# Kernel optimization log

Measured on AMD Instinct MI355X. Metric: run time of the kernel, lower is better.

Reference implementation:

```python
import jax, jax.numpy as jnp
import numpy as np

FEAT = 64
NSPIX = 256

def setup_inputs() -> dict:
    key = jax.random.key(0)
    ks = jax.random.split(key, 10)
    B, H, W = 8, 512, 512
    x = jax.random.normal(ks[0], (B, 3, H, W), dtype=jnp.float32)
    labels = jax.random.randint(ks[1], (B, 1, H, W), 0, NSPIX, dtype=jnp.int32)
    # learned params (1x1 convs as dense matrices, eval-mode BatchNorm stats)
    W_pix = jax.random.normal(ks[2], (FEAT, 3), dtype=jnp.float32) * 0.1
    b_pix = jax.random.normal(ks[3], (FEAT,), dtype=jnp.float32) * 0.01
    W_red = jax.random.normal(ks[4], (FEAT, 2 * FEAT), dtype=jnp.float32) * 0.05
    b_red = jax.random.normal(ks[5], (FEAT,), dtype=jnp.float32) * 0.01
    w_sim = jax.random.normal(ks[6], (1,), dtype=jnp.float32)
    b_sim = jax.random.normal(ks[7], (1,), dtype=jnp.float32) * 0.01
    bn_gamma = jnp.ones((1,), dtype=jnp.float32)
    bn_beta = jnp.zeros((1,), dtype=jnp.float32)
    bn_mean = jnp.zeros((1,), dtype=jnp.float32)
    bn_var = jnp.ones((1,), dtype=jnp.float32)
    return {"x": x, "labels": labels, "num_spixels": NSPIX,
            "W_pix": W_pix, "b_pix": b_pix, "W_red": W_red, "b_red": b_red,
            "w_sim": w_sim, "b_sim": b_sim,
            "bn_gamma": bn_gamma, "bn_beta": bn_beta,
            "bn_mean": bn_mean, "bn_var": bn_var}


def reference(x, labels, num_spixels, W_pix, b_pix, W_red, b_red,
              w_sim, b_sim, bn_gamma, bn_beta, bn_mean, bn_var):
    B, C, H, W = x.shape
    Fdim = W_pix.shape[0]
    # pixel_conv: 1x1 conv == per-pixel dense
    feats = jnp.einsum('fc,bchw->bfhw', W_pix, x) + b_pix[None, :, None, None]
    feats = feats.reshape(B, Fdim, H * W)              # [B, F, HW]
    lab = labels.reshape(B, H * W).astype(jnp.int32)   # [B, HW]
    # fused per-batch segment reduce: offset labels so one segment_sum handles all B
    seg = (lab + jnp.arange(B, dtype=jnp.int32)[:, None] * num_spixels).reshape(-1)
    nseg = B * num_spixels
    feat_flat = feats.transpose(0, 2, 1).reshape(-1, Fdim)       # [B*HW, F]
    count = jax.ops.segment_sum(jnp.ones((B * H * W,), dtype=feats.dtype), seg,
                                num_segments=nseg)
    count = jnp.maximum(count, 1.0).reshape(B, num_spixels, 1)    # [B, S, 1]
    ssum = jax.ops.segment_sum(feat_flat, seg, num_segments=nseg).reshape(B, num_spixels, Fdim)
    ssq = jax.ops.segment_sum(feat_flat * feat_flat, seg, num_segments=nseg).reshape(B, num_spixels, Fdim)
    mean = ssum / count                                           # [B, S, F]
    var = ssq / count - mean * mean
    std = jnp.sqrt(jnp.maximum(var, 1e-6))
    combined = jnp.concatenate([mean, std], axis=-1)              # [B, S, 2F]
    # reduce_conv: 1x1 conv over channel dim
    reduced = jnp.einsum('fg,bsg->bsf', W_red, combined) + b_red  # [B, S, F]
    # F.normalize(p=2, dim=channel) with eps=1e-12
    nrm = jnp.maximum(jnp.sqrt(jnp.sum(reduced * reduced, axis=-1, keepdims=True)), 1e-12)
    rn = reduced / nrm
    sim = jnp.einsum('bsf,btf->bst', rn, rn)                      # [B, S, S]
    # similarity_weight_block: Conv2d(1,1,1) -> BatchNorm2d(1, eval) -> ReLU
    y = sim * w_sim[0] + b_sim[0]
    y = bn_gamma[0] * (y - bn_mean[0]) / jnp.sqrt(bn_var[0] + 1e-5) + bn_beta[0]
    y = jax.nn.relu(y)
    return y[:, None, :, :]                                       # [B, 1, S, S]
```

## Files before the change

kernel.cpp:

```cpp
#include <hip/hip_runtime.h>

#define HW   262144
#define HW4  65536
#define NSEG 256
#define NB   8

__global__ __launch_bounds__(256) void k_moments(const float* __restrict__ x,
                                                 const int* __restrict__ labels,
                                                 float* __restrict__ part) {
  __shared__ unsigned cnt[NSEG];
  __shared__ unsigned offs[NSEG];
  __shared__ unsigned wtot[4];
  __shared__ __align__(16) float buf[2048][4];
  const int t = threadIdx.x, w = t >> 6, lane = t & 63;
  const int b = blockIdx.x >> 7, blk = blockIdx.x & 127;

  cnt[t] = 0u;
  __syncthreads();

  const float4* __restrict__ x4 = (const float4*)(x + (size_t)b * 3 * HW);
  const int4*  __restrict__ l4  = (const int4*)(labels + (size_t)b * HW);

  float4 A0[2], A1[2], A2[2];
  int lb[8];
  unsigned rk[8];

  #pragma unroll
  for (int it = 0; it < 2; ++it) {
    const int g = blk * 512 + w * 128 + it * 64 + lane;
    A0[it] = x4[g];
    A1[it] = x4[HW4 + g];
    A2[it] = x4[2 * HW4 + g];
    int4 lv = l4[g];
    lb[it * 4 + 0] = lv.x; lb[it * 4 + 1] = lv.y;
    lb[it * 4 + 2] = lv.z; lb[it * 4 + 3] = lv.w;
  }

  #pragma unroll
  for (int k = 0; k < 8; ++k) rk[k] = atomicAdd(&cnt[lb[k]], 1u);
  __syncthreads();

  const unsigned v = cnt[t];
  unsigned inc = v;
  #pragma unroll
  for (int off = 1; off < 64; off <<= 1) {
    unsigned u = __shfl_up(inc, off, 64);
    if (lane >= off) inc += u;
  }
  if (lane == 63) wtot[w] = inc;
  __syncthreads();
  unsigned wbase = 0;
  #pragma unroll
  for (int i = 0; i < 3; ++i) if (i < w) wbase += wtot[i];
  offs[t] = wbase + inc - v;
  __syncthreads();

  #pragma unroll
  for (int it = 0; it < 2; ++it) {
    float c0[4] = {A0[it].x, A0[it].y, A0[it].z, A0[it].w};
    float c1[4] = {A1[it].x, A1[it].y, A1[it].z, A1[it].w};
    float c2[4] = {A2[it].x, A2[it].y, A2[it].z, A2[it].w};
    #pragma unroll
    for (int k = 0; k < 4; ++k) {
      const int p = it * 4 + k;
      const unsigned pos = offs[lb[p]] + rk[p];
      *(float4*)&buf[pos][0] = make_float4(c0[k], c1[k], c2[k], 0.f);
    }
  }
  __syncthreads();

  const unsigned n = cnt[t], base = offs[t];
  float s0 = 0.f, s1 = 0.f, s2 = 0.f;
  float q00 = 0.f, q11 = 0.f, q22 = 0.f, q01 = 0.f, q02 = 0.f, q12 = 0.f;
  for (unsigned i = 0; i < n; ++i) {
    float4 p = *(const float4*)&buf[base + i][0];
    s0 += p.x;  s1 += p.y;  s2 += p.z;
    q00 += p.x * p.x;  q11 += p.y * p.y;  q22 += p.z * p.z;
    q01 += p.x * p.y;  q02 += p.x * p.z;  q12 += p.y * p.z;
  }

  float* o = part + (size_t)blockIdx.x * 2560;
  o[0 * NSEG + t] = (float)n;
  o[1 * NSEG + t] = s0;   o[2 * NSEG + t] = s1;   o[3 * NSEG + t] = s2;
  o[4 * NSEG + t] = q00;  o[5 * NSEG + t] = q11;  o[6 * NSEG + t] = q22;
  o[7 * NSEG + t] = q01;  o[8 * NSEG + t] = q02;  o[9 * NSEG + t] = q12;
}

__global__ __launch_bounds__(256) void k_reduce(const float* __restrict__ part,
                                                float* __restrict__ acc) {
  const int bm = blockIdx.x >> 2, c = blockIdx.x & 3;
  const int b = bm / 10, m = bm % 10;
  const float* p = part + ((size_t)(b * 128 + c * 32)) * 2560 + m * 256 + threadIdx.x;
  float s0 = 0.f, s1 = 0.f, s2 = 0.f, s3 = 0.f;
  for (int i = 0; i < 32; i += 4) {
    s0 += p[(size_t)(i + 0) * 2560];
    s1 += p[(size_t)(i + 1) * 2560];
    s2 += p[(size_t)(i + 2) * 2560];
    s3 += p[(size_t)(i + 3) * 2560];
  }
  acc[(size_t)((b * 4 + c) * 10 + m) * 256 + threadIdx.x] = (s0 + s1) + (s2 + s3);
}

__global__ __launch_bounds__(256) void k_stats(const float* __restrict__ acc,
                                               const float* __restrict__ W_pix,
                                               const float* __restrict__ b_pix,
                                               const float* __restrict__ W_red,
                                               const float* __restrict__ b_red,
                                               float* __restrict__ rn) {
  __shared__ float wred[64 * 129];
  __shared__ float comb[4][132];
  const int t = threadIdx.x;

  for (int j4 = t; j4 < 2048; j4 += 256) {
    const int row = j4 >> 5;
    const int c4  = (j4 & 31) << 2;
    float4 v = ((const float4*)W_red)[j4];
    float* d = &wred[row * 129 + c4];
    d[0] = v.x; d[1] = v.y; d[2] = v.z; d[3] = v.w;
  }
  __syncthreads();

  const int w = t >> 6;
  const int f = t & 63;
  const int seg = blockIdx.x * 4 + w;
  const int b = seg >> 8;
  const int s = seg & 255;

  float mm[10];
  #pragma unroll
  for (int m = 0; m < 10; ++m) {
    float v = 0.f;
    #pragma unroll
    for (int c = 0; c < 4; ++c)
      v += acc[(size_t)((b * 4 + c) * 10 + m) * 256 + s];
    mm[m] = v;
  }
  const float N   = fmaxf(mm[0], 1.0f);
  const float S0  = mm[1], S1 = mm[2], S2 = mm[3];
  const float M00 = mm[4], M11 = mm[5], M22 = mm[6];
  const float M01 = mm[7], M02 = mm[8], M12 = mm[9];

  const float w0 = W_pix[f * 3 + 0];
  const float w1 = W_pix[f * 3 + 1];
  const float w2 = W_pix[f * 3 + 2];
  const float bf = b_pix[f];

  const float wS   = w0 * S0 + w1 * S1 + w2 * S2;
  const float mean = (wS + N * bf) / N;
  const float ssq  = w0 * w0 * M00 + w1 * w1 * M11 + w2 * w2 * M22
                   + 2.f * (w0 * w1 * M01 + w0 * w2 * M02 + w1 * w2 * M12)
                   + 2.f * bf * wS + N * bf * bf;
  const float var  = ssq / N - mean * mean;
  const float stdv = sqrtf(fmaxf(var, 1e-6f));

  comb[w][f]      = mean;
  comb[w][64 + f] = stdv;
  __syncthreads();

  float r = b_red[f];
  const float* wr = &wred[f * 129];
  const float* cb = comb[w];
  for (int g = 0; g < 128; ++g) r += wr[g] * cb[g];

  float sq = r * r;
  #pragma unroll
  for (int off = 32; off > 0; off >>= 1) sq += __shfl_xor(sq, off, 64);
  const float inv = 1.0f / fmaxf(sqrtf(sq), 1e-12f);

  rn[(size_t)seg * 64 + f] = r * inv;
}

__global__ __launch_bounds__(256) void k_sim(const float* __restrict__ rn,
                                             float* __restrict__ out,
                                             const float* __restrict__ w_sim,
                                             const float* __restrict__ b_sim,
                                             const float* __restrict__ bn_g,
                                             const float* __restrict__ bn_b,
                                             const float* __restrict__ bn_m,
                                             const float* __restrict__ bn_v) {
  __shared__ float A[64 * 65];
  __shared__ float Bt[64 * 65];
  const int t  = threadIdx.x;
  const int b  = blockIdx.x >> 4;
  const int ti = (blockIdx.x >> 2) & 3;
  const int tj = blockIdx.x & 3;

  const float4* rn4 = (const float4*)(rn + (size_t)b * NSEG * 64);
  for (int j4 = t; j4 < 1024; j4 += 256) {
    const int row = j4 >> 4;
    const int c4  = (j4 & 15) << 2;
    float4 va = rn4[(ti * 64 + row) * 16 + (j4 & 15)];
    float* da = &A[row * 65 + c4];
    da[0] = va.x; da[1] = va.y; da[2] = va.z; da[3] = va.w;
    float4 vb = rn4[(tj * 64 + row) * 16 + (j4 & 15)];
    float* db = &Bt[row * 65 + c4];
    db[0] = vb.x; db[1] = vb.y; db[2] = vb.z; db[3] = vb.w;
  }
  __syncthreads();

  const int tx = t & 15;
  const int ty = t >> 4;
  float acc[4][4] = {{0.f}};
  for (int k = 0; k < 64; ++k) {
    float av[4], bv[4];
    #pragma unroll
    for (int i = 0; i < 4; ++i) av[i] = A[(ty * 4 + i) * 65 + k];
    #pragma unroll
    for (int j = 0; j < 4; ++j) bv[j] = Bt[(tx * 4 + j) * 65 + k];
    #pragma unroll
    for (int i = 0; i < 4; ++i)
      #pragma unroll
      for (int j = 0; j < 4; ++j) acc[i][j] += av[i] * bv[j];
  }

  const float invsd = 1.0f / sqrtf(bn_v[0] + 1e-5f);
  const float scale = w_sim[0] * bn_g[0] * invsd;
  const float shift = (b_sim[0] - bn_m[0]) * bn_g[0] * invsd + bn_b[0];

  #pragma unroll
  for (int i = 0; i < 4; ++i) {
    float4 v;
    v.x = fmaxf(acc[i][0] * scale + shift, 0.f);
    v.y = fmaxf(acc[i][1] * scale + shift, 0.f);
    v.z = fmaxf(acc[i][2] * scale + shift, 0.f);
    v.w = fmaxf(acc[i][3] * scale + shift, 0.f);
    const int base = b * 65536 + (ti * 64 + ty * 4 + i) * 256 + tj * 64;
    ((float4*)out)[(base >> 2) + tx] = v;
  }
}

extern "C" void kernel_launch(void* const* d_in, const int* in_sizes, int n_in,
                              void* d_out, int out_size, void* d_ws, size_t ws_size,
                              hipStream_t stream) {
  (void)in_sizes; (void)n_in; (void)out_size; (void)ws_size;
  const float* x      = (const float*)d_in[0];
  const int*   labels = (const int*)d_in[1];
  const float* W_pix  = (const float*)d_in[3];
  const float* b_pix  = (const float*)d_in[4];
  const float* W_red  = (const float*)d_in[5];
  const float* b_red  = (const float*)d_in[6];
  const float* w_sim  = (const float*)d_in[7];
  const float* b_sim  = (const float*)d_in[8];
  const float* bn_g   = (const float*)d_in[9];
  const float* bn_b   = (const float*)d_in[10];
  const float* bn_m   = (const float*)d_in[11];
  const float* bn_v   = (const float*)d_in[12];
  float* out = (float*)d_out;

  float* part = (float*)d_ws;
  float* acc  = part + (size_t)1024 * 2560;
  float* rn   = acc + NB * 4 * 10 * NSEG;

  k_moments<<<dim3(1024), dim3(256), 0, stream>>>(x, labels, part);
  k_reduce<<<dim3(320), dim3(256), 0, stream>>>(part, acc);
  k_stats<<<dim3(512), dim3(256), 0, stream>>>(acc, W_pix, b_pix, W_red, b_red, rn);
  k_sim<<<dim3(128), dim3(256), 0, stream>>>(rn, out, w_sim, b_sim, bn_g, bn_b, bn_m, bn_v);
}
```

Measured before the change: 114.5 us.

## Replace LDS atomic histogram with wave ballot match-any ranking; split k_sim tiles

The counting sort in k_moments no longer uses per-pixel LDS atomicAdd. Each wave computes per-label ranks with 8 ballots (a match-any), writes per-(wave,slot) group counts into a 16-bit histogram in shared memory, and prefix-scans those counts to get scatter positions. This shared buffer is reused later as the float4 sort buffer. The moment accumulation loop is unrolled by two, and k_sim switches to 32-row tiles with 256 blocks for better CU coverage. The ballot path adds many ALU/ballot operations per pixel and extra syncs in exchange for avoiding atomic contention.

```diff
diff --git a/kernel.cpp b/kernel.cpp
--- a/kernel.cpp
+++ b/kernel.cpp
@@ -11,19 +11,18 @@
   __shared__ unsigned cnt[NSEG];
   __shared__ unsigned offs[NSEG];
   __shared__ unsigned wtot[4];
-  __shared__ __align__(16) float buf[2048][4];
+  __shared__ __align__(16) char smem[32768];
+  unsigned short (*gh)[NSEG] = (unsigned short(*)[NSEG])smem;
+  float4* buf = (float4*)smem;
+
   const int t = threadIdx.x, w = t >> 6, lane = t & 63;
   const int b = blockIdx.x >> 7, blk = blockIdx.x & 127;
 
-  cnt[t] = 0u;
-  __syncthreads();
-
   const float4* __restrict__ x4 = (const float4*)(x + (size_t)b * 3 * HW);
   const int4*  __restrict__ l4  = (const int4*)(labels + (size_t)b * HW);
 
   float4 A0[2], A1[2], A2[2];
   int lb[8];
-  unsigned rk[8];
 
   #pragma unroll
   for (int it = 0; it < 2; ++it) {
@@ -36,11 +35,42 @@
     lb[it * 4 + 2] = lv.z; lb[it * 4 + 3] = lv.w;
   }
 
-  #pragma unroll
-  for (int k = 0; k < 8; ++k) rk[k] = atomicAdd(&cnt[lb[k]], 1u);
-  __syncthreads();
-
-  const unsigned v = cnt[t];
+  unsigned* z = (unsigned*)smem;
+  #pragma unroll
+  for (int i = 0; i < 16; ++i) z[t + 256 * i] = 0u;
+  __syncthreads();
+
+  const unsigned long long below = (1ull << lane) - 1ull;
+  unsigned rk[8];
+  #pragma unroll
+  for (int k = 0; k < 8; ++k) {
+    const int l = lb[k];
+    unsigned long long m = ~0ull;
+    #pragma unroll
+    for (int bit = 0; bit < 8; ++bit) {
+      const unsigned long long bal = __ballot((l >> bit) & 1);
+      m &= ((l >> bit) & 1) ? bal : ~bal;
+    }
+    rk[k] = (unsigned)__popcll(m & below);
+    if (rk[k] == 0) gh[w * 8 + k][l] = (unsigned short)__popcll(m);
+  }
+  __syncthreads();
+
+  unsigned run = 0;
+  #pragma unroll
+  for (int r = 0; r < 4; ++r) {
+    unsigned vv[8];
+    #pragma unroll
+    for (int j = 0; j < 8; ++j) vv[j] = gh[r * 8 + j][t];
+    #pragma unroll
+    for (int j = 0; j < 8; ++j) {
+      gh[r * 8 + j][t] = (unsigned short)run;
+      run += vv[j];
+    }
+  }
+  cnt[t] = run;
+
+  const unsigned v = run;
   unsigned inc = v;
   #pragma unroll
   for (int off = 1; off < 64; off <<= 1) {
@@ -53,6 +83,12 @@
   #pragma unroll
   for (int i = 0; i < 3; ++i) if (i < w) wbase += wtot[i];
   offs[t] = wbase + inc - v;
+  __syncthreads();
+
+  unsigned pos[8];
+  #pragma unroll
+  for (int k = 0; k < 8; ++k)
+    pos[k] = offs[lb[k]] + (unsigned)gh[w * 8 + k][lb[k]] + rk[k];
   __syncthreads();
 
   #pragma unroll
@@ -61,19 +97,28 @@
     float c1[4] = {A1[it].x, A1[it].y, A1[it].z, A1[it].w};
     float c2[4] = {A2[it].x, A2[it].y, A2[it].z, A2[it].w};
     #pragma unroll
-    for (int k = 0; k < 4; ++k) {
-      const int p = it * 4 + k;
-      const unsigned pos = offs[lb[p]] + rk[p];
-      *(float4*)&buf[pos][0] = make_float4(c0[k], c1[k], c2[k], 0.f);
-    }
+    for (int k = 0; k < 4; ++k)
+      buf[pos[it * 4 + k]] = make_float4(c0[k], c1[k], c2[k], 0.f);
   }
   __syncthreads();
 
   const unsigned n = cnt[t], base = offs[t];
   float s0 = 0.f, s1 = 0.f, s2 = 0.f;
   float q00 = 0.f, q11 = 0.f, q22 = 0.f, q01 = 0.f, q02 = 0.f, q12 = 0.f;
-  for (unsigned i = 0; i < n; ++i) {
-    float4 p = *(const float4*)&buf[base + i][0];
+  unsigned i = 0;
+  for (; i + 2 <= n; i += 2) {
+    float4 p = buf[base + i];
+    float4 q = buf[base + i + 1];
+    s0 += p.x + q.x;  s1 += p.y + q.y;  s2 += p.z + q.z;
+    q00 += p.x * p.x + q.x * q.x;
+    q11 += p.y * p.y + q.y * q.y;
+    q22 += p.z * p.z + q.z * q.z;
+    q01 += p.x * p.y + q.x * q.y;
+    q02 += p.x * p.z + q.x * q.z;
+    q12 += p.y * p.z + q.y * q.z;
+  }
+  if (i < n) {
+    float4 p = buf[base + i];
     s0 += p.x;  s1 += p.y;  s2 += p.z;
     q00 += p.x * p.x;  q11 += p.y * p.y;  q22 += p.z * p.z;
     q01 += p.x * p.y;  q02 += p.x * p.z;  q12 += p.y * p.z;
@@ -178,20 +223,22 @@
                                              const float* __restrict__ bn_b,
                                              const float* __restrict__ bn_m,
                                              const float* __restrict__ bn_v) {
-  __shared__ float A[64 * 65];
+  __shared__ float A[32 * 65];
   __shared__ float Bt[64 * 65];
   const int t  = threadIdx.x;
-  const int b  = blockIdx.x >> 4;
-  const int ti = (blockIdx.x >> 2) & 3;
+  const int b  = blockIdx.x >> 5;
+  const int ti = (blockIdx.x >> 2) & 7;
   const int tj = blockIdx.x & 3;
 
   const float4* rn4 = (const float4*)(rn + (size_t)b * NSEG * 64);
   for (int j4 = t; j4 < 1024; j4 += 256) {
     const int row = j4 >> 4;
     const int c4  = (j4 & 15) << 2;
-    float4 va = rn4[(ti * 64 + row) * 16 + (j4 & 15)];
-    float* da = &A[row * 65 + c4];
-    da[0] = va.x; da[1] = va.y; da[2] = va.z; da[3] = va.w;
+    if (j4 < 512) {
+      float4 va = rn4[(ti * 32 + row) * 16 + (j4 & 15)];
+      float* da = &A[row * 65 + c4];
+      da[0] = va.x; da[1] = va.y; da[2] = va.z; da[3] = va.w;
+    }
     float4 vb = rn4[(tj * 64 + row) * 16 + (j4 & 15)];
     float* db = &Bt[row * 65 + c4];
     db[0] = vb.x; db[1] = vb.y; db[2] = vb.z; db[3] = vb.w;
@@ -200,15 +247,15 @@
 
   const int tx = t & 15;
   const int ty = t >> 4;
-  float acc[4][4] = {{0.f}};
+  float acc[2][4] = {{0.f}};
   for (int k = 0; k < 64; ++k) {
-    float av[4], bv[4];
-    #pragma unroll
-    for (int i = 0; i < 4; ++i) av[i] = A[(ty * 4 + i) * 65 + k];
+    float av[2], bv[4];
+    #pragma unroll
+    for (int i = 0; i < 2; ++i) av[i] = A[(ty * 2 + i) * 65 + k];
     #pragma unroll
     for (int j = 0; j < 4; ++j) bv[j] = Bt[(tx * 4 + j) * 65 + k];
     #pragma unroll
-    for (int i = 0; i < 4; ++i)
+    for (int i = 0; i < 2; ++i)
       #pragma unroll
       for (int j = 0; j < 4; ++j) acc[i][j] += av[i] * bv[j];
   }
@@ -218,13 +265,13 @@
   const float shift = (b_sim[0] - bn_m[0]) * bn_g[0] * invsd + bn_b[0];
 
   #pragma unroll
-  for (int i = 0; i < 4; ++i) {
+  for (int i = 0; i < 2; ++i) {
     float4 v;
     v.x = fmaxf(acc[i][0] * scale + shift, 0.f);
     v.y = fmaxf(acc[i][1] * scale + shift, 0.f);
     v.z = fmaxf(acc[i][2] * scale + shift, 0.f);
     v.w = fmaxf(acc[i][3] * scale + shift, 0.f);
-    const int base = b * 65536 + (ti * 64 + ty * 4 + i) * 256 + tj * 64;
+    const int base = b * 65536 + (ti * 32 + ty * 2 + i) * 256 + tj * 64;
     ((float4*)out)[(base >> 2) + tx] = v;
   }
 }
@@ -254,5 +301,5 @@
   k_moments<<<dim3(1024), dim3(256), 0, stream>>>(x, labels, part);
   k_reduce<<<dim3(320), dim3(256), 0, stream>>>(part, acc);
   k_stats<<<dim3(512), dim3(256), 0, stream>>>(acc, W_pix, b_pix, W_red, b_red, rn);
-  k_sim<<<dim3(128), dim3(256), 0, stream>>>(rn, out, w_sim, b_sim, bn_g, bn_b, bn_m, bn_v);
-}
+  k_sim<<<dim3(256), dim3(256), 0, stream>>>(rn, out, w_sim, b_sim, bn_g, bn_b, bn_m, bn_v);
+}
```

Result: no change. 116.6 us (+1.8%).
